# Optimization experiments

Hardware: AMD Instinct MI355X
Metric: run time of the kernel (lower is better)

The kernel has to match this reference:

```python
import jax, jax.numpy as jnp
import numpy as np

SPAN_MAX_LEN = 8
BUCKET_BINS = np.array([0, 1, 2, 3, 4, 5, 7, 8, 15, 16, 31, 32, 63, 64], dtype=np.int64)


def _span_indices(L, max_len):
    # all contiguous spans of width 1..min(L, max_len), grouped by width (matches torch unfold order)
    starts, ends = [], []
    for w in range(1, min(L, max_len) + 1):
        s = np.arange(0, L - w + 1, dtype=np.int64)
        starts.append(s)
        ends.append(s + w - 1)
    return np.concatenate(starts), np.concatenate(ends)


def setup_inputs() -> dict:
    key = jax.random.key(0)
    k1, k2 = jax.random.split(key)
    B, L, D, W = 16, 128, 768, 128
    x = jax.random.normal(k1, (B, L, D), dtype=jnp.float32)
    width_embedding = jax.random.normal(k2, (len(BUCKET_BINS), W), dtype=jnp.float32)
    return {"x": x, "width_embedding": width_embedding, "batch_max_seq_len": L}


def reference(x, width_embedding, batch_max_seq_len):
    B = x.shape[0]
    starts, ends = _span_indices(int(batch_max_seq_len), SPAN_MAX_LEN)  # static np arrays
    widths = ends - starts + 1
    # bucket = last index where width >= bin  ==  searchsorted(side='right') - 1
    buckets = np.searchsorted(BUCKET_BINS, widths, side="right") - 1  # [n_spans]
    n_spans = starts.shape[0]
    hi = x[:, starts, :]                                   # [B, n_spans, D]
    hj = x[:, ends, :]                                     # [B, n_spans, D]
    fw = jnp.broadcast_to(width_embedding[buckets][None, :, :],
                          (B, n_spans, width_embedding.shape[1]))
    spans = jnp.concatenate([hi, hj, fw], axis=-1)         # [B, n_spans, 2D+W]
    span_indices = jnp.stack([jnp.asarray(starts), jnp.asarray(ends)], axis=-1)
    return spans, span_indices
```

## Files before the change

### kernel.cpp

```cpp
#include <hip/hip_runtime.h>


#define LSEQ    128
#define DDIM    768
#define WDIM    128
#define NSPANS  996
#define ROW     1664
#define ROW4    416
#define PER_B4  (NSPANS * ROW4)
#define IDX4    498
#define NWG_MAIN 25896

typedef float f4 __attribute__((ext_vector_type(4)));

__device__ __forceinline__ void decode_span(int s, int& start, int& end, int& bucket) {
    int w = 1, base = 0;
    if (s >= 128) { w = 2; base = 128; }
    if (s >= 255) { w = 3; base = 255; }
    if (s >= 381) { w = 4; base = 381; }
    if (s >= 506) { w = 5; base = 506; }
    if (s >= 630) { w = 6; base = 630; }
    if (s >= 753) { w = 7; base = 753; }
    if (s >= 875) { w = 8; base = 875; }
    start  = s - base;
    end    = start + w - 1;
    bucket = w - (w >= 6 ? 1 : 0);
}

__global__ __launch_bounds__(256) void span_rep_kernel(
        const float* __restrict__ x,
        const float* __restrict__ we,
        float* __restrict__ out) {
    const int wg = blockIdx.x;

    if (wg < NWG_MAIN) {
        const int xcd = wg & 7;
        const int j   = wg >> 3;
        const int idx = j * 256 + threadIdx.x;
        const int half = (idx >= PER_B4) ? 1 : 0;
        const int b    = 2 * xcd + half;
        const int rem  = idx - half * PER_B4;
        const int s    = rem / ROW4;
        const int c4   = rem - s * ROW4;
        const int c    = c4 * 4;

        int start, end, bucket;
        decode_span(s, start, end, bucket);

        f4 v;
        if (c < DDIM) {
            v = *reinterpret_cast<const f4*>(
                    &x[((long)b * LSEQ + start) * DDIM + c]);
        } else if (c < 2 * DDIM) {
            v = *reinterpret_cast<const f4*>(
                    &x[((long)b * LSEQ + end) * DDIM + (c - DDIM)]);
        } else {
            v = *reinterpret_cast<const f4*>(
                    &we[bucket * WDIM + (c - 2 * DDIM)]);
        }
        const long i = (long)b * PER_B4 + rem;
        *reinterpret_cast<f4*>(&out[i * 4]) = v;
    } else {
        const int k = (wg - NWG_MAIN) * 256 + threadIdx.x;
        if (k < IDX4) {
            int s0 = 2 * k, s1 = 2 * k + 1;
            int st0, en0, bk0, st1, en1, bk1;
            decode_span(s0, st0, en0, bk0);
            decode_span(s1, st1, en1, bk1);
            f4 v = { (float)st0, (float)en0, (float)st1, (float)en1 };
            *reinterpret_cast<f4*>(&out[(long)NWG_MAIN * 1024 + (long)k * 4]) = v;
        }
    }
}

extern "C" void kernel_launch(void* const* d_in, const int* in_sizes, int n_in,
                              void* d_out, int out_size, void* d_ws, size_t ws_size,
                              hipStream_t stream) {
    const float* x  = (const float*)d_in[0];
    const float* we = (const float*)d_in[1];
    float* out = (float*)d_out;

    const int grid = NWG_MAIN + 2;
    span_rep_kernel<<<grid, 256, 0, stream>>>(x, we, out);
}
```

Measured before the change: 22.55 us.

## Scatter each input row to all its span slots instead of gathering per output

The work is inverted from an output-centric gather to an input-centric scatter. Each wave loads one x row chunk once and writes it to up to 16 output positions (start and end slots for widths 1..8). The width-embedding segment gets its own block range. This cuts redundant global reads and per-element span decoding, but the writes become strided scatters across distant rows, which may hurt write coalescing and locality.

```diff
diff --git a/kernel.cpp b/kernel.cpp
--- a/kernel.cpp
+++ b/kernel.cpp
@@ -1,19 +1,34 @@
 #include <hip/hip_runtime.h>
 
 
-#define LSEQ    128
-#define DDIM    768
-#define WDIM    128
-#define NSPANS  996
-#define ROW     1664
-#define ROW4    416
-#define PER_B4  (NSPANS * ROW4)
-#define IDX4    498
-#define NWG_MAIN 25896
+#define LSEQ   128
+#define DDIM   768
+#define NSPANS 996
+#define ROW    1664
+#define PER_B  ((long)NSPANS * ROW)
+#define XPART_BLOCKS 1536
+#define FW_BLOCKS    1992
+#define FWTOT        509952
+#define IDX4         498
+#define SPANS_FLOATS ((long)16 * PER_B)
 
 typedef float f4 __attribute__((ext_vector_type(4)));
 
-__device__ __forceinline__ void decode_span(int s, int& start, int& end, int& bucket) {
+__device__ __constant__ int kBase[8] = {0, 128, 255, 381, 506, 630, 753, 875};
+
+__device__ __forceinline__ int bucket_of_span(int s) {
+    int w = 1;
+    if (s >= 128) w = 2;
+    if (s >= 255) w = 3;
+    if (s >= 381) w = 4;
+    if (s >= 506) w = 5;
+    if (s >= 630) w = 6;
+    if (s >= 753) w = 7;
+    if (s >= 875) w = 8;
+    return w - (w >= 6 ? 1 : 0);
+}
+
+__device__ __forceinline__ void start_end_of_span(int s, int& start, int& end) {
     int w = 1, base = 0;
     if (s >= 128) { w = 2; base = 128; }
     if (s >= 255) { w = 3; base = 255; }
@@ -22,9 +37,8 @@
     if (s >= 630) { w = 6; base = 630; }
     if (s >= 753) { w = 7; base = 753; }
     if (s >= 875) { w = 8; base = 875; }
-    start  = s - base;
-    end    = start + w - 1;
-    bucket = w - (w >= 6 ? 1 : 0);
+    start = s - base;
+    end   = start + w - 1;
 }
 
 __global__ __launch_bounds__(256) void span_rep_kernel(
@@ -33,42 +47,53 @@
         float* __restrict__ out) {
     const int wg = blockIdx.x;
 
-    if (wg < NWG_MAIN) {
-        const int xcd = wg & 7;
-        const int j   = wg >> 3;
-        const int idx = j * 256 + threadIdx.x;
-        const int half = (idx >= PER_B4) ? 1 : 0;
+    if (wg < XPART_BLOCKS) {
+        const int xcd  = wg & 7;
+        const int jj   = wg >> 3;
+        const int wave = threadIdx.x >> 6;
+        const int lane = threadIdx.x & 63;
+        const int gw   = jj * 4 + wave;
+        const int half = (gw >= 384) ? 1 : 0;
         const int b    = 2 * xcd + half;
-        const int rem  = idx - half * PER_B4;
-        const int s    = rem / ROW4;
-        const int c4   = rem - s * ROW4;
-        const int c    = c4 * 4;
+        const int r    = gw - half * 384;
+        const int s    = r / 3;
+        const int q    = r - s * 3;
+        const int c    = (q * 64 + lane) * 4;
 
-        int start, end, bucket;
-        decode_span(s, start, end, bucket);
+        const f4 v = *reinterpret_cast<const f4*>(
+            &x[((long)b * LSEQ + s) * DDIM + c]);
 
-        f4 v;
-        if (c < DDIM) {
-            v = *reinterpret_cast<const f4*>(
-                    &x[((long)b * LSEQ + start) * DDIM + c]);
-        } else if (c < 2 * DDIM) {
-            v = *reinterpret_cast<const f4*>(
-                    &x[((long)b * LSEQ + end) * DDIM + (c - DDIM)]);
-        } else {
-            v = *reinterpret_cast<const f4*>(
-                    &we[bucket * WDIM + (c - 2 * DDIM)]);
+        float* ob = out + (long)b * PER_B;
+
+        #pragma unroll
+        for (int w = 1; w <= 8; ++w) {
+            const int base = (w==1)?0:(w==2)?128:(w==3)?255:(w==4)?381:
+                             (w==5)?506:(w==6)?630:(w==7)?753:875;
+            if (s <= LSEQ - w) {
+                *reinterpret_cast<f4*>(&ob[(long)(base + s) * ROW + c]) = v;
+            }
+            if (s >= w - 1) {
+                *reinterpret_cast<f4*>(&ob[(long)(base + s - w + 1) * ROW + DDIM + c]) = v;
+            }
         }
-        const long i = (long)b * PER_B4 + rem;
-        *reinterpret_cast<f4*>(&out[i * 4]) = v;
+    } else if (wg < XPART_BLOCKS + FW_BLOCKS) {
+        const int f = (wg - XPART_BLOCKS) * 256 + (int)threadIdx.x;
+        const int b    = f / 31872;
+        const int rem  = f - b * 31872;
+        const int sIdx = rem >> 5;
+        const int c4f  = rem & 31;
+        const int bucket = bucket_of_span(sIdx);
+        const f4 v = *reinterpret_cast<const f4*>(&we[bucket * 128 + c4f * 4]);
+        *reinterpret_cast<f4*>(
+            &out[(long)b * PER_B + (long)sIdx * ROW + 2 * DDIM + c4f * 4]) = v;
     } else {
-        const int k = (wg - NWG_MAIN) * 256 + threadIdx.x;
+        const int k = (wg - XPART_BLOCKS - FW_BLOCKS) * 256 + (int)threadIdx.x;
         if (k < IDX4) {
-            int s0 = 2 * k, s1 = 2 * k + 1;
-            int st0, en0, bk0, st1, en1, bk1;
-            decode_span(s0, st0, en0, bk0);
-            decode_span(s1, st1, en1, bk1);
+            int st0, en0, st1, en1;
+            start_end_of_span(2 * k,     st0, en0);
+            start_end_of_span(2 * k + 1, st1, en1);
             f4 v = { (float)st0, (float)en0, (float)st1, (float)en1 };
-            *reinterpret_cast<f4*>(&out[(long)NWG_MAIN * 1024 + (long)k * 4]) = v;
+            *reinterpret_cast<f4*>(&out[SPANS_FLOATS + (long)k * 4]) = v;
         }
     }
 }
@@ -80,6 +105,6 @@
     const float* we = (const float*)d_in[1];
     float* out = (float*)d_out;
 
-    const int grid = NWG_MAIN + 2;
+    const int grid = XPART_BLOCKS + FW_BLOCKS + 2;
     span_rep_kernel<<<grid, 256, 0, stream>>>(x, we, out);
 }
```

After: 22.17 us. No clear change (-1.7%).
